# Optimization experiments

Hardware: AMD Instinct MI355X
Metric: run time of the kernel (lower is better)

The kernel has to match this reference:

```python
import jax, jax.numpy as jnp
import numpy as np

B, T, D, H, F = 2, 2048, 2048, 16, 8192
DH = D // H  # 128
EPS = 1e-6   # flax LayerNorm default


def _layernorm(x, scale, bias):
    mu = jnp.mean(x, axis=-1, keepdims=True)
    var = jnp.mean(jnp.square(x - mu), axis=-1, keepdims=True)
    return (x - mu) * jax.lax.rsqrt(var + EPS) * scale + bias


def setup_inputs() -> dict:
    key = jax.random.key(0)
    ks = jax.random.split(key, 8)
    w = 0.02
    return {
        "x": jax.random.normal(ks[0], (B, T, D), jnp.float32),
        "ln1_scale": jnp.ones((D,), jnp.float32),
        "ln1_bias": jnp.zeros((D,), jnp.float32),
        "w_qkv": jax.random.normal(ks[1], (D, 3 * D), jnp.float32) * w,
        "b_qkv": jnp.zeros((3 * D,), jnp.float32),
        "ln2_scale": jnp.ones((D,), jnp.float32),
        "ln2_bias": jnp.zeros((D,), jnp.float32),
        "w1": jax.random.normal(ks[2], (D, F), jnp.float32) * w,
        "b1": jnp.zeros((F,), jnp.float32),
        "w2": jax.random.normal(ks[3], (F, D), jnp.float32) * w,
        "b2": jnp.zeros((D,), jnp.float32),
    }


def reference(x, ln1_scale, ln1_bias, w_qkv, b_qkv, ln2_scale, ln2_bias, w1, b1, w2, b2):
    # --- pre-LN causal self-attention (training=False -> dropout = identity) ---
    r = _layernorm(x, ln1_scale, ln1_bias)
    qkv = r @ w_qkv + b_qkv                       # [B,T,3D]
    q, k, v = jnp.split(qkv, 3, axis=-1)
    q = q.reshape(B, T, H, DH)
    k = k.reshape(B, T, H, DH)
    v = v.reshape(B, T, H, DH)
    attn = jnp.einsum('bthd,bThd->bhtT', q, k) / jnp.sqrt(jnp.float32(DH))
    causal = jnp.tril(jnp.ones((T, T), bool))
    attn = jnp.where(causal, attn, -jnp.inf)
    attn = jax.nn.softmax(attn, axis=-1)
    out = jnp.einsum('bhtT,bThd->bthd', attn, v).reshape(B, T, D)
    # NOTE: original module has no output projection after attention.
    x = x + out
    # --- MLP block ---
    r = _layernorm(x, ln2_scale, ln2_bias)
    h = jax.nn.gelu(r @ w1 + b1, approximate=True)  # flax nn.gelu default
    x = x + (h @ w2 + b2)
    return x
```

## Files before the change

kernel.cpp:

```cpp
#include <hip/hip_runtime.h>
#include <hip/hip_bf16.h>
#include <stdint.h>
#include <stddef.h>

using bf16_t = __hip_bfloat16;
typedef __attribute__((ext_vector_type(8))) short short8;
typedef __attribute__((ext_vector_type(4))) float f32x4;

__device__ __forceinline__ void gload_lds16(const void* g, void* l) {
  __builtin_amdgcn_global_load_lds((const __attribute__((address_space(1))) void*)g,
                                   (__attribute__((address_space(3))) void*)l,
                                   16, 0, 0);
}

__global__ __launch_bounds__(256) void k_transpose_cvt(const float* __restrict__ in,
                                                       bf16_t* __restrict__ out,
                                                       int K, int N) {
  __shared__ float tile[64][65];
  int n0 = blockIdx.x * 64, k0 = blockIdx.y * 64;
  int t = threadIdx.x;
#pragma unroll
  for (int i = 0; i < 16; ++i) {
    int idx = t + i * 256;
    int kk = idx >> 6, nn = idx & 63;
    tile[kk][nn] = in[(size_t)(k0 + kk) * N + n0 + nn];
  }
  __syncthreads();
#pragma unroll
  for (int i = 0; i < 16; ++i) {
    int idx = t + i * 256;
    int nn = idx >> 6, kk = idx & 63;
    out[(size_t)(n0 + nn) * K + k0 + kk] = __float2bfloat16(tile[kk][nn]);
  }
}

__global__ __launch_bounds__(256) void k_layernorm(const float* __restrict__ x,
                                                   const float* __restrict__ gam,
                                                   const float* __restrict__ bet,
                                                   bf16_t* __restrict__ out) {
  int row = blockIdx.x, t = threadIdx.x;
  const float4* xr = (const float4*)(x + (size_t)row * 2048);
  float4 a = xr[t], b = xr[t + 256];
  float s  = a.x + a.y + a.z + a.w + b.x + b.y + b.z + b.w;
  float s2 = a.x*a.x + a.y*a.y + a.z*a.z + a.w*a.w
           + b.x*b.x + b.y*b.y + b.z*b.z + b.w*b.w;
#pragma unroll
  for (int off = 32; off >= 1; off >>= 1) {
    s  += __shfl_xor(s, off);
    s2 += __shfl_xor(s2, off);
  }
  __shared__ float red[8];
  if ((t & 63) == 0) { red[t >> 6] = s; red[4 + (t >> 6)] = s2; }
  __syncthreads();
  float S  = red[0] + red[1] + red[2] + red[3];
  float S2 = red[4] + red[5] + red[6] + red[7];
  float mu = S * (1.0f / 2048.0f);
  float var = S2 * (1.0f / 2048.0f) - mu * mu;
  float rstd = rsqrtf(var + 1e-6f);
  const float4* gv = (const float4*)gam;
  const float4* bv = (const float4*)bet;
  float4 g1 = gv[t], g2 = gv[t + 256], c1 = bv[t], c2 = bv[t + 256];
  bf16_t* orow = out + (size_t)row * 2048;
  orow[4*t + 0]    = __float2bfloat16((a.x - mu) * rstd * g1.x + c1.x);
  orow[4*t + 1]    = __float2bfloat16((a.y - mu) * rstd * g1.y + c1.y);
  orow[4*t + 2]    = __float2bfloat16((a.z - mu) * rstd * g1.z + c1.z);
  orow[4*t + 3]    = __float2bfloat16((a.w - mu) * rstd * g1.w + c1.w);
  orow[1024 + 4*t + 0] = __float2bfloat16((b.x - mu) * rstd * g2.x + c2.x);
  orow[1024 + 4*t + 1] = __float2bfloat16((b.y - mu) * rstd * g2.y + c2.y);
  orow[1024 + 4*t + 2] = __float2bfloat16((b.z - mu) * rstd * g2.z + c2.z);
  orow[1024 + 4*t + 3] = __float2bfloat16((b.w - mu) * rstd * g2.w + c2.w);
}

template <int EPI>
__global__ __launch_bounds__(512, 2) void k_gemm8(const bf16_t* __restrict__ A,
                                                  const bf16_t* __restrict__ Bt,
                                                  const float* __restrict__ bias,
                                                  bf16_t* __restrict__ Cb,
                                                  float* __restrict__ Cf,
                                                  int Ndim, int LDA, int LDB,
                                                  int Kdim, int nkch) {
  __shared__ __align__(16) char lds[131072];
  int nwg = gridDim.x;
  int orig = blockIdx.x;
  int wg = (orig & 7) * (nwg >> 3) + (orig >> 3);
  int bpc = nwg / nkch;
  int chunk = wg / bpc;
  int rem = wg - chunk * bpc;
  int m0 = (rem & 15) * 256;
  int n0 = (rem >> 4) * 256;
  int tid = threadIdx.x;
  int w = tid >> 6, lane = tid & 63;
  int lr = lane & 15, lk = lane >> 4;
  int wr = w >> 2, wc = w & 3;

  const bf16_t* Ag = A + (size_t)m0 * LDA + (size_t)chunk * Kdim;
  const bf16_t* Bg = Bt + (size_t)n0 * LDB + (size_t)chunk * Kdim;
  int swch = ((tid & 7) ^ ((tid >> 3) & 7)) << 3;
  const bf16_t* pA0 = Ag + (size_t)(tid >> 3) * LDA + swch;
  const bf16_t* pA1 = pA0 + (size_t)128 * LDA;
  int nb0 = ((tid >> 8) & 1) * 64 + ((tid >> 3) & 31);
  const bf16_t* pB0 = Bg + (size_t)nb0 * LDB + swch;
  const bf16_t* pB1 = pB0 + (size_t)128 * LDB;
  int dstb = tid * 16;
  int chv0 = ((lk)     ^ (lr & 7)) * 16;
  int chv1 = ((4 + lk) ^ (lr & 7)) * 16;
  int aof0 = 65536 + wr * 8192 + lr * 128 + chv0;
  int aof1 = 65536 + wr * 8192 + lr * 128 + chv1;
  int bof0 = wc * 4096 + lr * 128 + chv0;
  int bof1 = wc * 4096 + lr * 128 + chv1;

  f32x4 acc[8][4];
#pragma unroll
  for (int i = 0; i < 8; ++i)
#pragma unroll
    for (int j = 0; j < 4; ++j) acc[i][j] = (f32x4){0.f, 0.f, 0.f, 0.f};
  short8 af[4][2], bq[2][2];

#define STAGE_A(p, h, kt) do { \
    size_t ko = (size_t)(kt) * 64 + (size_t)(h) * 64 * LDA; \
    gload_lds16(pA0 + ko, lds + 65536 + (p) * 32768 + (h) * 16384 + dstb); \
    gload_lds16(pA1 + ko, lds + 65536 + (p) * 32768 + (h) * 16384 + 8192 + dstb); } while (0)
#define STAGE_B(p, h, kt) do { \
    size_t ko = (size_t)(kt) * 64 + (size_t)(h) * 32 * LDB; \
    gload_lds16(pB0 + ko, lds + (p) * 32768 + (h) * 16384 + dstb); \
    gload_lds16(pB1 + ko, lds + (p) * 32768 + (h) * 16384 + 8192 + dstb); } while (0)
#define READ_A(p, mh) do { \
    _Pragma("unroll") for (int mf = 0; mf < 4; ++mf) { \
      af[mf][0] = *(const short8*)(lds + (p) * 32768 + (mh) * 16384 + mf * 2048 + aof0); \
      af[mf][1] = *(const short8*)(lds + (p) * 32768 + (mh) * 16384 + mf * 2048 + aof1); } } while (0)
#define READ_B(p, nh) do { \
    _Pragma("unroll") for (int nf = 0; nf < 2; ++nf) { \
      bq[nf][0] = *(const short8*)(lds + (p) * 32768 + (nh) * 16384 + nf * 2048 + bof0); \
      bq[nf][1] = *(const short8*)(lds + (p) * 32768 + (nh) * 16384 + nf * 2048 + bof1); } } while (0)
#define MM16(mh, nh) do { \
    _Pragma("unroll") for (int ks = 0; ks < 2; ++ks) \
    _Pragma("unroll") for (int mf = 0; mf < 4; ++mf) \
    _Pragma("unroll") for (int nf = 0; nf < 2; ++nf) \
      acc[(mh) * 4 + mf][(nh) * 2 + nf] = __builtin_amdgcn_mfma_f32_16x16x32_bf16( \
          af[mf][ks], bq[nf][ks], acc[(mh) * 4 + mf][(nh) * 2 + nf], 0, 0, 0); } while (0)
#define BARRIER() asm volatile("s_barrier" ::: "memory")
#define LGKM0()  do { asm volatile("s_waitcnt lgkmcnt(0)" ::: "memory"); __builtin_amdgcn_sched_barrier(0); } while (0)
#define PRIO1()  __builtin_amdgcn_s_setprio(1)
#define PRIO0()  __builtin_amdgcn_s_setprio(0)
#define BODY(t, p, S1, S2, VMN) do { \
    READ_A(p, 0); READ_B(p, 0); \
    if (S1) STAGE_B((p) ^ 1, 0, (t) + 1); \
    asm volatile("s_waitcnt lgkmcnt(8)" ::: "memory"); \
    BARRIER(); LGKM0(); PRIO1(); MM16(0, 0); PRIO0(); BARRIER(); \
    READ_B(p, 1); \
    if (S2) STAGE_A(p, 0, (t) + 2); \
    BARRIER(); LGKM0(); PRIO1(); MM16(0, 1); PRIO0(); BARRIER(); \
    READ_A(p, 1); \
    if (S2) STAGE_B(p, 1, (t) + 2); \
    BARRIER(); LGKM0(); PRIO1(); MM16(1, 1); PRIO0(); BARRIER(); \
    READ_B(p, 0); \
    if (S2) STAGE_A(p, 1, (t) + 2); \
    BARRIER(); LGKM0(); PRIO1(); MM16(1, 0); PRIO0(); \
    asm volatile("s_waitcnt vmcnt(%0)" :: "i"(VMN) : "memory"); \
    BARRIER(); } while (0)

  const int NT = Kdim >> 6;
  STAGE_A(0, 0, 0); STAGE_B(0, 0, 0); STAGE_B(0, 1, 0); STAGE_A(0, 1, 0);
  STAGE_A(1, 0, 1); STAGE_B(1, 1, 1); STAGE_A(1, 1, 1);
  asm volatile("s_waitcnt vmcnt(6)" ::: "memory");
  BARRIER();

  int t = 0;
  for (; t + 3 < NT; t += 2) {
    BODY(t, 0, 1, 1, 6);
    BODY(t + 1, 1, 1, 1, 6);
  }
  BODY(t, 0, 1, 0, 0);
  {
    READ_A(1, 0); READ_B(1, 0);
    BARRIER(); LGKM0(); MM16(0, 0); BARRIER();
    READ_B(1, 1);
    BARRIER(); LGKM0(); MM16(0, 1); BARRIER();
    READ_A(1, 1);
    BARRIER(); LGKM0(); MM16(1, 1); BARRIER();
    READ_B(1, 0);
    LGKM0(); MM16(1, 0);
  }
#undef STAGE_A
#undef STAGE_B
#undef READ_A
#undef READ_B
#undef MM16
#undef BARRIER
#undef LGKM0
#undef PRIO1
#undef PRIO0
#undef BODY

#pragma unroll
  for (int mf = 0; mf < 8; ++mf) {
#pragma unroll
    for (int nf = 0; nf < 4; ++nf) {
#pragma unroll
      for (int r = 0; r < 4; ++r) {
        int rw = m0 + wr * 128 + mf * 16 + lk * 4 + r;
        int cl = n0 + wc * 64 + nf * 16 + lr;
        float v = acc[mf][nf][r];
        size_t gi = (size_t)rw * Ndim + cl;
        if (EPI == 0) {
          Cb[gi] = __float2bfloat16(v + bias[cl]);
        } else if (EPI == 1) {
          float vv = v + bias[cl];
          float u = vv * (vv * vv * 0.044715f + 1.0f) * 0.7978845608028654f;
          float gl = 0.5f * vv * (1.0f + tanhf(u));
          Cb[gi] = __float2bfloat16(gl);
        } else {
          float add = v + (chunk == 0 ? bias[cl] : 0.0f);
          atomicAdd(&Cf[gi], add);
        }
      }
    }
  }
}

__global__ __launch_bounds__(256) void k_transpose_v(const bf16_t* __restrict__ qkv,
                                                     bf16_t* __restrict__ vT) {
  __shared__ bf16_t tile[64][72];
  int bid = blockIdx.x;
  int tt = bid & 31;
  int dt = (bid >> 5) & 1;
  int h  = (bid >> 6) & 15;
  int b  = bid >> 10;
  int t0 = tt * 64, d0 = dt * 64;
  int t = threadIdx.x;
  const bf16_t* src = qkv + (size_t)(b * 2048) * 6144 + 4096 + h * 128;
#pragma unroll
  for (int i = 0; i < 16; ++i) {
    int idx = t + i * 256;
    int rr = idx >> 6, cc = idx & 63;
    tile[rr][cc] = src[(size_t)(t0 + rr) * 6144 + d0 + cc];
  }
  __syncthreads();
  bf16_t* dst = vT + (size_t)(b * 16 + h) * 128 * 2048;
#pragma unroll
  for (int i = 0; i < 16; ++i) {
    int idx = t + i * 256;
    int rr = idx >> 6, cc = idx & 63;
    dst[(size_t)(d0 + rr) * 2048 + t0 + cc] = tile[cc][rr];
  }
}

__global__ __launch_bounds__(256, 2) void k_attn(const bf16_t* __restrict__ qkv,
                                                 const bf16_t* __restrict__ vT,
                                                 const float* __restrict__ x,
                                                 float* __restrict__ out) {
  __shared__ __align__(16) bf16_t Pl[4][32][40];
  int j = blockIdx.x;
  int bh = j & 31;
  int cq = j >> 5;
  int b = bh >> 4, h = bh & 15;
  int w = threadIdx.x >> 6, lane = threadIdx.x & 63;
  int lr = lane & 15, lk = lane >> 4;
  int c = (w == 0) ? cq : (w == 1) ? (63 - cq) : (w == 2) ? (31 - cq) : (32 + cq);
  int q0 = c * 32;
  const bf16_t* qb = qkv + (size_t)(b * 2048) * 6144 + h * 128;
  const bf16_t* kb = qb + 2048;
  const bf16_t* vb = vT + (size_t)(b * 16 + h) * 128 * 2048;
  short8 qf[2][4];
#pragma unroll
  for (int qg = 0; qg < 2; ++qg)
#pragma unroll
    for (int d4 = 0; d4 < 4; ++d4)
      qf[qg][d4] = *(const short8*)(qb + (size_t)(q0 + qg * 16 + lr) * 6144 + d4 * 32 + lk * 8);
  float m[2][4], l[2][4];
#pragma unroll
  for (int qg = 0; qg < 2; ++qg)
#pragma unroll
    for (int r = 0; r < 4; ++r) { m[qg][r] = -1e30f; l[qg][r] = 0.f; }
  f32x4 o[2][8] = {};
  int nkt = c + 1;
  const float sc = 0.08838834764831845f;
  for (int kt = 0; kt < nkt; ++kt) {
    int tk0 = kt * 32;
    short8 vf[8];
#pragma unroll
    for (int d8 = 0; d8 < 8; ++d8)
      vf[d8] = *(const short8*)(vb + (size_t)(d8 * 16 + lr) * 2048 + tk0 + lk * 8);
    short8 kf[2][4];
#pragma unroll
    for (int nt = 0; nt < 2; ++nt)
#pragma unroll
      for (int d4 = 0; d4 < 4; ++d4)
        kf[nt][d4] = *(const short8*)(kb + (size_t)(tk0 + nt * 16 + lr) * 6144 + d4 * 32 + lk * 8);
    f32x4 s[2][2] = {};
#pragma unroll
    for (int d4 = 0; d4 < 4; ++d4)
#pragma unroll
      for (int qg = 0; qg < 2; ++qg)
#pragma unroll
        for (int nt = 0; nt < 2; ++nt)
          s[qg][nt] = __builtin_amdgcn_mfma_f32_16x16x32_bf16(qf[qg][d4], kf[nt][d4], s[qg][nt], 0, 0, 0);
#pragma unroll
    for (int qg = 0; qg < 2; ++qg) {
      float sv[2][4], mt[4];
#pragma unroll
      for (int r = 0; r < 4; ++r) {
        int qr = q0 + qg * 16 + lk * 4 + r;
#pragma unroll
        for (int nt = 0; nt < 2; ++nt) {
          float v = s[qg][nt][r] * sc;
          int kc = tk0 + nt * 16 + lr;
          sv[nt][r] = (kc > qr) ? -1e30f : v;
        }
        mt[r] = fmaxf(sv[0][r], sv[1][r]);
      }
#pragma unroll
      for (int off = 1; off < 16; off <<= 1)
#pragma unroll
        for (int r = 0; r < 4; ++r) mt[r] = fmaxf(mt[r], __shfl_xor(mt[r], off));
      float alpha[4], rs[4];
#pragma unroll
      for (int r = 0; r < 4; ++r) {
        float mn = fmaxf(m[qg][r], mt[r]);
        alpha[r] = __expf(m[qg][r] - mn);
        m[qg][r] = mn;
      }
#pragma unroll
      for (int r = 0; r < 4; ++r) {
        float p0 = __expf(sv[0][r] - m[qg][r]);
        float p1 = __expf(sv[1][r] - m[qg][r]);
        rs[r] = p0 + p1;
        Pl[w][qg * 16 + lk * 4 + r][lr]      = __float2bfloat16(p0);
        Pl[w][qg * 16 + lk * 4 + r][16 + lr] = __float2bfloat16(p1);
      }
#pragma unroll
      for (int off = 1; off < 16; off <<= 1)
#pragma unroll
        for (int r = 0; r < 4; ++r) rs[r] += __shfl_xor(rs[r], off);
#pragma unroll
      for (int r = 0; r < 4; ++r) l[qg][r] = l[qg][r] * alpha[r] + rs[r];
#pragma unroll
      for (int d8 = 0; d8 < 8; ++d8)
#pragma unroll
        for (int r = 0; r < 4; ++r) o[qg][d8][r] *= alpha[r];
    }
    asm volatile("s_waitcnt lgkmcnt(0)" ::: "memory");
    short8 pf[2];
#pragma unroll
    for (int qg = 0; qg < 2; ++qg)
      pf[qg] = *(const short8*)(&Pl[w][qg * 16 + lr][lk * 8]);
#pragma unroll
    for (int d8 = 0; d8 < 8; ++d8)
#pragma unroll
      for (int qg = 0; qg < 2; ++qg)
        o[qg][d8] = __builtin_amdgcn_mfma_f32_16x16x32_bf16(pf[qg], vf[d8], o[qg][d8], 0, 0, 0);
  }
#pragma unroll
  for (int qg = 0; qg < 2; ++qg)
#pragma unroll
    for (int d8 = 0; d8 < 8; ++d8)
#pragma unroll
      for (int r = 0; r < 4; ++r) {
        int qr = q0 + qg * 16 + lk * 4 + r;
        int cl = h * 128 + d8 * 16 + lr;
        size_t gi = (size_t)(b * 2048 + qr) * 2048 + cl;
        out[gi] = x[gi] + o[qg][d8][r] / l[qg][r];
      }
}

extern "C" void kernel_launch(void* const* d_in, const int* in_sizes, int n_in,
                              void* d_out, int out_size, void* d_ws, size_t ws_size,
                              hipStream_t stream) {
  const float* x    = (const float*)d_in[0];
  const float* ln1s = (const float*)d_in[1];
  const float* ln1b = (const float*)d_in[2];
  const float* wqkv = (const float*)d_in[3];
  const float* bqkv = (const float*)d_in[4];
  const float* ln2s = (const float*)d_in[5];
  const float* ln2b = (const float*)d_in[6];
  const float* w1   = (const float*)d_in[7];
  const float* b1   = (const float*)d_in[8];
  const float* w2   = (const float*)d_in[9];
  const float* b2   = (const float*)d_in[10];
  float* out = (float*)d_out;
  char* ws = (char*)d_ws;

  bf16_t* r     = (bf16_t*)(ws + 0);
  bf16_t* vT    = (bf16_t*)(ws + 0);
  bf16_t* qkv   = (bf16_t*)(ws + 16777216);
  bf16_t* w1T   = (bf16_t*)(ws + 67108864);
  bf16_t* w2T   = (bf16_t*)(ws + 100663296);
  bf16_t* h     = (bf16_t*)(ws + 134217728);
  bf16_t* wqkvT = (bf16_t*)(ws + 134217728);

  k_transpose_cvt<<<dim3(96, 32),  256, 0, stream>>>(wqkv, wqkvT, 2048, 6144);
  k_transpose_cvt<<<dim3(128, 32), 256, 0, stream>>>(w1,   w1T,   2048, 8192);
  k_transpose_cvt<<<dim3(32, 128), 256, 0, stream>>>(w2,   w2T,   8192, 2048);
  k_layernorm<<<4096, 256, 0, stream>>>(x, ln1s, ln1b, r);
  k_gemm8<0><<<384, 512, 0, stream>>>(r, wqkvT, bqkv, qkv, nullptr, 6144, 2048, 2048, 2048, 1);
  k_transpose_v<<<2048, 256, 0, stream>>>(qkv, vT);
  k_attn<<<512, 256, 0, stream>>>(qkv, vT, x, out);
  k_layernorm<<<4096, 256, 0, stream>>>(out, ln2s, ln2b, r);
  k_gemm8<1><<<512, 512, 0, stream>>>(r, w1T, b1, h, nullptr, 8192, 2048, 2048, 2048, 1);
  k_gemm8<3><<<256, 512, 0, stream>>>(h, w2T, b2, nullptr, out, 2048, 8192, 8192, 4096, 2);
}
```

Before: 658.6 us.

## Vectorize weight transpose, remap GEMM tiles per XCD, prefetch K/V in attention

```diff
diff --git a/kernel.cpp b/kernel.cpp
--- a/kernel.cpp
+++ b/kernel.cpp
@@ -5,6 +5,7 @@
 
 using bf16_t = __hip_bfloat16;
 typedef __attribute__((ext_vector_type(8))) short short8;
+typedef __attribute__((ext_vector_type(4))) short short4v;
 typedef __attribute__((ext_vector_type(4))) float f32x4;
 
 __device__ __forceinline__ void gload_lds16(const void* g, void* l) {
@@ -19,18 +20,25 @@
   __shared__ float tile[64][65];
   int n0 = blockIdx.x * 64, k0 = blockIdx.y * 64;
   int t = threadIdx.x;
-#pragma unroll
-  for (int i = 0; i < 16; ++i) {
-    int idx = t + i * 256;
-    int kk = idx >> 6, nn = idx & 63;
-    tile[kk][nn] = in[(size_t)(k0 + kk) * N + n0 + nn];
+  int tr = t >> 4, tc = t & 15;
+#pragma unroll
+  for (int i = 0; i < 4; ++i) {
+    float4 v = *(const float4*)(in + (size_t)(k0 + tr + i * 16) * N + n0 + tc * 4);
+    tile[tr + i * 16][tc * 4 + 0] = v.x;
+    tile[tr + i * 16][tc * 4 + 1] = v.y;
+    tile[tr + i * 16][tc * 4 + 2] = v.z;
+    tile[tr + i * 16][tc * 4 + 3] = v.w;
   }
   __syncthreads();
 #pragma unroll
-  for (int i = 0; i < 16; ++i) {
-    int idx = t + i * 256;
-    int nn = idx >> 6, kk = idx & 63;
-    out[(size_t)(n0 + nn) * K + k0 + kk] = __float2bfloat16(tile[kk][nn]);
+  for (int i = 0; i < 4; ++i) {
+    int nn = tr + i * 16;
+    short4v s;
+    s[0] = (short)__bfloat16_as_ushort(__float2bfloat16(tile[tc * 4 + 0][nn]));
+    s[1] = (short)__bfloat16_as_ushort(__float2bfloat16(tile[tc * 4 + 1][nn]));
+    s[2] = (short)__bfloat16_as_ushort(__float2bfloat16(tile[tc * 4 + 2][nn]));
+    s[3] = (short)__bfloat16_as_ushort(__float2bfloat16(tile[tc * 4 + 3][nn]));
+    *(short4v*)(out + (size_t)(n0 + nn) * K + k0 + tc * 4) = s;
   }
 }
 
@@ -78,16 +86,17 @@
                                                   bf16_t* __restrict__ Cb,
                                                   float* __restrict__ Cf,
                                                   int Ndim, int LDA, int LDB,
-                                                  int Kdim, int nkch) {
+                                                  int Kdim, int nsub) {
   __shared__ __align__(16) char lds[131072];
-  int nwg = gridDim.x;
   int orig = blockIdx.x;
-  int wg = (orig & 7) * (nwg >> 3) + (orig >> 3);
-  int bpc = nwg / nkch;
-  int chunk = wg / bpc;
-  int rem = wg - chunk * bpc;
-  int m0 = (rem & 15) * 256;
-  int n0 = (rem >> 4) * 256;
+  int xcd = orig & 7;
+  int i = orig >> 3;
+  int m = i & 15;
+  int j = i >> 4;
+  int n_local = j % nsub;
+  int chunk = j / nsub;
+  int m0 = m * 256;
+  int n0 = (xcd * nsub + n_local) * 256;
   int tid = threadIdx.x;
   int w = tid >> 6, lane = tid & 63;
   int lr = lane & 15, lk = lane >> 4;
@@ -111,9 +120,9 @@
 
   f32x4 acc[8][4];
 #pragma unroll
-  for (int i = 0; i < 8; ++i)
-#pragma unroll
-    for (int j = 0; j < 4; ++j) acc[i][j] = (f32x4){0.f, 0.f, 0.f, 0.f};
+  for (int ii = 0; ii < 8; ++ii)
+#pragma unroll
+    for (int jj = 0; jj < 4; ++jj) acc[ii][jj] = (f32x4){0.f, 0.f, 0.f, 0.f};
   short8 af[4][2], bq[2][2];
 
 #define STAGE_A(p, h, kt) do { \
@@ -275,19 +284,20 @@
   f32x4 o[2][8] = {};
   int nkt = c + 1;
   const float sc = 0.08838834764831845f;
+  short8 kf[2][4], vf[8];
+#pragma unroll
+  for (int nt = 0; nt < 2; ++nt)
+#pragma unroll
+    for (int d4 = 0; d4 < 4; ++d4)
+      kf[nt][d4] = *(const short8*)(kb + (size_t)(nt * 16 + lr) * 6144 + d4 * 32 + lk * 8);
+#pragma unroll
+  for (int d8 = 0; d8 < 8; ++d8)
+    vf[d8] = *(const short8*)(vb + (size_t)(d8 * 16 + lr) * 2048 + lk * 8);
+
   for (int kt = 0; kt < nkt; ++kt) {
     int tk0 = kt * 32;
-    short8 vf[8];
-#pragma unroll
-    for (int d8 = 0; d8 < 8; ++d8)
-      vf[d8] = *(const short8*)(vb + (size_t)(d8 * 16 + lr) * 2048 + tk0 + lk * 8);
-    short8 kf[2][4];
-#pragma unroll
-    for (int nt = 0; nt < 2; ++nt)
-#pragma unroll
-      for (int d4 = 0; d4 < 4; ++d4)
-        kf[nt][d4] = *(const short8*)(kb + (size_t)(tk0 + nt * 16 + lr) * 6144 + d4 * 32 + lk * 8);
     f32x4 s[2][2] = {};
+    __builtin_amdgcn_s_setprio(1);
 #pragma unroll
     for (int d4 = 0; d4 < 4; ++d4)
 #pragma unroll
@@ -295,6 +305,15 @@
 #pragma unroll
         for (int nt = 0; nt < 2; ++nt)
           s[qg][nt] = __builtin_amdgcn_mfma_f32_16x16x32_bf16(qf[qg][d4], kf[nt][d4], s[qg][nt], 0, 0, 0);
+    __builtin_amdgcn_s_setprio(0);
+    if (kt + 1 < nkt) {
+      int tn = tk0 + 32;
+#pragma unroll
+      for (int nt = 0; nt < 2; ++nt)
+#pragma unroll
+        for (int d4 = 0; d4 < 4; ++d4)
+          kf[nt][d4] = *(const short8*)(kb + (size_t)(tn + nt * 16 + lr) * 6144 + d4 * 32 + lk * 8);
+    }
 #pragma unroll
     for (int qg = 0; qg < 2; ++qg) {
       float sv[2][4], mt[4];
@@ -344,11 +363,19 @@
 #pragma unroll
     for (int qg = 0; qg < 2; ++qg)
       pf[qg] = *(const short8*)(&Pl[w][qg * 16 + lr][lk * 8]);
+    __builtin_amdgcn_s_setprio(1);
 #pragma unroll
     for (int d8 = 0; d8 < 8; ++d8)
 #pragma unroll
       for (int qg = 0; qg < 2; ++qg)
         o[qg][d8] = __builtin_amdgcn_mfma_f32_16x16x32_bf16(pf[qg], vf[d8], o[qg][d8], 0, 0, 0);
+    __builtin_amdgcn_s_setprio(0);
+    if (kt + 1 < nkt) {
+      int tn = tk0 + 32;
+#pragma unroll
+      for (int d8 = 0; d8 < 8; ++d8)
+        vf[d8] = *(const short8*)(vb + (size_t)(d8 * 16 + lr) * 2048 + tn + lk * 8);
+    }
   }
 #pragma unroll
   for (int qg = 0; qg < 2; ++qg)
@@ -392,10 +419,10 @@
   k_transpose_cvt<<<dim3(128, 32), 256, 0, stream>>>(w1,   w1T,   2048, 8192);
   k_transpose_cvt<<<dim3(32, 128), 256, 0, stream>>>(w2,   w2T,   8192, 2048);
   k_layernorm<<<4096, 256, 0, stream>>>(x, ln1s, ln1b, r);
-  k_gemm8<0><<<384, 512, 0, stream>>>(r, wqkvT, bqkv, qkv, nullptr, 6144, 2048, 2048, 2048, 1);
+  k_gemm8<0><<<384, 512, 0, stream>>>(r, wqkvT, bqkv, qkv, nullptr, 6144, 2048, 2048, 2048, 3);
   k_transpose_v<<<2048, 256, 0, stream>>>(qkv, vT);
   k_attn<<<512, 256, 0, stream>>>(qkv, vT, x, out);
   k_layernorm<<<4096, 256, 0, stream>>>(out, ln2s, ln2b, r);
-  k_gemm8<1><<<512, 512, 0, stream>>>(r, w1T, b1, h, nullptr, 8192, 2048, 2048, 2048, 1);
-  k_gemm8<3><<<256, 512, 0, stream>>>(h, w2T, b2, nullptr, out, 2048, 8192, 8192, 4096, 2);
-}
+  k_gemm8<1><<<512, 512, 0, stream>>>(r, w1T, b1, h, nullptr, 8192, 2048, 2048, 2048, 4);
+  k_gemm8<3><<<256, 512, 0, stream>>>(h, w2T, b2, nullptr, out, 2048, 8192, 8192, 4096, 1);
+}
```

New measurement: 656.4 us. About the same (-0.3%).
